# Kernel tuning notes

Hardware: AMD Instinct MI355X
Metric: run time of the kernel (lower is better)

The kernel has to match this reference:

```python
import jax, jax.numpy as jnp
import numpy as np

B, NUM_FRAMES, NUM_PATCHES = 2, 16, 196
DIM, H, DH = 768, 12, 64
T = NUM_FRAMES * NUM_PATCHES  # 3136
EPS = 1e-5


def setup_inputs() -> dict:
    key = jax.random.key(0)
    ks = jax.random.split(key, 5)
    x = jax.random.normal(ks[0], (B, T, DIM), jnp.float32)
    context = jax.random.normal(ks[1], (B, T, DIM), jnp.float32)
    Wq = jax.random.normal(ks[2], (DIM, H * DH), jnp.float32) * 0.02
    Wkv = jax.random.normal(ks[3], (DIM, 2 * H * DH), jnp.float32) * 0.02
    Wo = jax.random.normal(ks[4], (H * DH, DIM), jnp.float32) * 0.02
    bo = jnp.zeros((DIM,), jnp.float32)
    gamma = jnp.ones((DIM,), jnp.float32)
    beta = jnp.zeros((DIM,), jnp.float32)
    # block-diagonal frame mask: patch i attends to patch j iff same frame
    frame_ids = jnp.arange(T) // NUM_PATCHES
    mask = frame_ids[:, None] == frame_ids[None, :]  # [T, T] bool
    return {"x": x, "context": context, "Wq": Wq, "Wkv": Wkv, "Wo": Wo,
            "bo": bo, "gamma": gamma, "beta": beta, "mask": mask}


def reference(x, context, Wq, Wkv, Wo, bo, gamma, beta, mask):
    # LayerNorm on queries only (torch LN: biased variance, eps=1e-5)
    mu = jnp.mean(x, axis=-1, keepdims=True)
    var = jnp.var(x, axis=-1, keepdims=True)
    xn = (x - mu) * jax.lax.rsqrt(var + EPS) * gamma + beta

    q = xn @ Wq                      # [B, T, H*DH]
    kv = context @ Wkv               # [B, T, 2*H*DH]
    k, v = jnp.split(kv, 2, axis=-1)

    def split_heads(t):
        return t.reshape(B, T, H, DH).transpose(0, 2, 1, 3)  # [B, H, T, DH]

    q, k, v = split_heads(q), split_heads(k), split_heads(v)

    scale = DH ** -0.5
    dots = jnp.einsum('bhnd,bhmd->bhnm', q, k) * scale      # [B, H, T, T]
    dots = jnp.where(mask, dots, -jnp.inf)
    attn = jax.nn.softmax(dots, axis=-1)                    # dropout p=0.0 -> identity
    out = jnp.einsum('bhnm,bhmd->bhnd', attn, v)            # [B, H, T, DH]
    out = out.transpose(0, 2, 1, 3).reshape(B, T, H * DH)
    return out @ Wo + bo
```

## Files before the change

kernel.cpp:

```cpp
#include <hip/hip_runtime.h>
#include <hip/hip_bf16.h>

#define NB 2
#define TT 3136
#define DIM 768
#define NH 12
#define NF 16
#define NP 196

typedef __attribute__((ext_vector_type(8))) short short8;
typedef __attribute__((ext_vector_type(4))) short s16x4;
typedef __attribute__((ext_vector_type(4))) float f32x4;
typedef unsigned int uint;

__device__ __forceinline__ float bf2f(short s) {
    return __uint_as_float(((uint)(unsigned short)s) << 16);
}
__device__ __forceinline__ short f2bs(float f) {
    __hip_bfloat16 h = __float2bfloat16(f);
    short s; __builtin_memcpy(&s, &h, 2); return s;
}
__device__ __forceinline__ void load16_lds(const void* g, void* l) {
    __builtin_amdgcn_global_load_lds(
        (const __attribute__((address_space(1))) unsigned int*)g,
        (__attribute__((address_space(3))) unsigned int*)l, 16, 0, 0);
}

__global__ __launch_bounds__(256)
void prep_w(const float* __restrict__ Wq, const float* __restrict__ Wkv,
            const float* __restrict__ Wo,
            __hip_bfloat16* __restrict__ WqT, __hip_bfloat16* __restrict__ WkvT,
            __hip_bfloat16* __restrict__ WoT) {
    __shared__ float tile[32][33];
    int bx = blockIdx.x;
    const float* W; __hip_bfloat16* WT; int N, n0;
    if (bx < 24)      { W = Wq;  WT = WqT;  N = DIM;     n0 = bx * 32; }
    else if (bx < 72) { W = Wkv; WT = WkvT; N = 2 * DIM; n0 = (bx - 24) * 32; }
    else              { W = Wo;  WT = WoT;  N = DIM;     n0 = (bx - 72) * 32; }
    int k0 = blockIdx.y * 32;
    int tx = threadIdx.x & 31, ty = threadIdx.x >> 5;
#pragma unroll
    for (int i = 0; i < 32; i += 8)
        tile[ty + i][tx] = W[(size_t)(k0 + ty + i) * N + (n0 + tx)];
    __syncthreads();
#pragma unroll
    for (int i = 0; i < 32; i += 8)
        WT[(size_t)(n0 + ty + i) * DIM + (k0 + tx)] = __float2bfloat16(tile[tx][ty + i]);
}

__global__ __launch_bounds__(256)
void prep_xc(const float* __restrict__ ctx, __hip_bfloat16* __restrict__ cb,
             const float* __restrict__ x, const float* __restrict__ gamma,
             const float* __restrict__ beta, __hip_bfloat16* __restrict__ xn) {
    int blk = blockIdx.x, tid = threadIdx.x;
    if (blk < 4704) {
        size_t i = (size_t)blk * 256 + tid;
        f32x4 f; __builtin_memcpy(&f, ctx + i * 4, 16);
        s16x4 s;
#pragma unroll
        for (int j = 0; j < 4; j++) s[j] = f2bs(f[j]);
        __builtin_memcpy((short*)cb + i * 4, &s, 8);
        return;
    }
    int row = blk - 4704;
    const float* xr = x + (size_t)row * DIM;
    float v[3], s = 0.f, ss = 0.f;
#pragma unroll
    for (int i = 0; i < 3; i++) {
        v[i] = xr[tid + i * 256];
        s += v[i]; ss += v[i] * v[i];
    }
#pragma unroll
    for (int off = 32; off; off >>= 1) {
        s += __shfl_xor(s, off);
        ss += __shfl_xor(ss, off);
    }
    __shared__ float red[8];
    int wid = tid >> 6, lane = tid & 63;
    if (lane == 0) { red[wid] = s; red[wid + 4] = ss; }
    __syncthreads();
    if (tid == 0) {
        float S = red[0] + red[1] + red[2] + red[3];
        float SS = red[4] + red[5] + red[6] + red[7];
        float mu = S / DIM;
        float var = SS / DIM - mu * mu;
        red[0] = mu;
        red[1] = rsqrtf(var + 1e-5f);
    }
    __syncthreads();
    float mu = red[0], rs = red[1];
#pragma unroll
    for (int i = 0; i < 3; i++) {
        int c = tid + i * 256;
        xn[(size_t)row * DIM + c] = __float2bfloat16((v[i] - mu) * rs * gamma[c] + beta[c]);
    }
}

__global__ __launch_bounds__(256)
void gemm_qkv(const __hip_bfloat16* __restrict__ xn,
              const __hip_bfloat16* __restrict__ cb,
              const __hip_bfloat16* __restrict__ WqT,
              const __hip_bfloat16* __restrict__ WkvT,
              __hip_bfloat16* __restrict__ qbuf,
              __hip_bfloat16* __restrict__ kvbuf) {
    __shared__ short sA[2][128 * 64];
    __shared__ short sB[2][128 * 64];
    int orig = blockIdx.x;
    int xcd = orig & 7, pos = orig >> 3;
    int wgid = (xcd < 2 ? xcd * 111 : 222 + (xcd - 2) * 110) + pos;
    int mt = wgid / 18, nt = wgid - mt * 18;
    const __hip_bfloat16 *A, *BT;
    __hip_bfloat16* C;
    int N, n0;
    if (nt < 6) { A = xn; BT = WqT;  C = qbuf;  N = DIM;     n0 = nt * 128; }
    else        { A = cb; BT = WkvT; C = kvbuf; N = 2 * DIM; n0 = (nt - 6) * 128; }
    int m0 = mt * 128;
    int tid = threadIdx.x, lane = tid & 63, wave = tid >> 6;
    int r = lane & 15, q = lane >> 4;
    int wm = (wave & 1) * 64, wn = (wave >> 1) * 64;
    f32x4 acc[4][4] = {};

    auto stage = [&](int buf, int k0) {
#pragma unroll
        for (int i = 0; i < 4; i++) {
            int c = i * 256 + tid;
            int row = c >> 3, cg = c & 7;
            load16_lds(A + (size_t)(m0 + row) * DIM + k0 + cg * 8, &sA[buf][c * 8]);
        }
#pragma unroll
        for (int i = 0; i < 4; i++) {
            int c = i * 256 + tid;
            int row = c >> 3, cg = c & 7;
            load16_lds(BT + (size_t)(n0 + row) * DIM + k0 + cg * 8, &sB[buf][c * 8]);
        }
    };
    auto compute = [&](int buf) {
#pragma unroll
        for (int ks = 0; ks < 2; ks++) {
            short8 af[4], bfv[4];
#pragma unroll
            for (int t = 0; t < 4; t++) {
                __builtin_memcpy(&af[t],  &sA[buf][(wm + t * 16 + r) * 64 + ks * 32 + q * 8], 16);
                __builtin_memcpy(&bfv[t], &sB[buf][(wn + t * 16 + r) * 64 + ks * 32 + q * 8], 16);
            }
            __builtin_amdgcn_s_setprio(1);
#pragma unroll
            for (int mi = 0; mi < 4; mi++)
#pragma unroll
                for (int ni = 0; ni < 4; ni++)
                    acc[mi][ni] = __builtin_amdgcn_mfma_f32_16x16x32_bf16(
                        af[mi], bfv[ni], acc[mi][ni], 0, 0, 0);
            __builtin_amdgcn_s_setprio(0);
        }
    };

    stage(0, 0);
    __syncthreads();
    int cur = 0;
#pragma unroll 2
    for (int t = 0; t < 11; ++t) {
        stage(cur ^ 1, (t + 1) * 64);
        compute(cur);
        __syncthreads();
        cur ^= 1;
    }
    compute(cur);

#pragma unroll
    for (int mi = 0; mi < 4; mi++)
#pragma unroll
        for (int ni = 0; ni < 4; ni++)
#pragma unroll
            for (int rr = 0; rr < 4; rr++) {
                int row = m0 + wm + mi * 16 + q * 4 + rr;
                int col = n0 + wn + ni * 16 + r;
                C[(size_t)row * N + col] = __float2bfloat16(acc[mi][ni][rr]);
            }
}

__global__ __launch_bounds__(256)
void gemm_o(const __hip_bfloat16* __restrict__ A,
            const __hip_bfloat16* __restrict__ BT,
            const float* __restrict__ bias,
            float* __restrict__ C) {
    __shared__ short sA[2][128 * 64];
    __shared__ short sB[2][128 * 64];
    int orig = blockIdx.x;
    int xcd = orig & 7, pos = orig >> 3;
    int wgid = (xcd < 6 ? xcd * 37 : 222 + (xcd - 6) * 36) + pos;
    int mt = wgid / 6, nt = wgid - mt * 6;
    int m0 = mt * 128, n0 = nt * 128;
    int tid = threadIdx.x, lane = tid & 63, wave = tid >> 6;
    int r = lane & 15, q = lane >> 4;
    int wm = (wave & 1) * 64, wn = (wave >> 1) * 64;
    f32x4 acc[4][4] = {};

    auto stage = [&](int buf, int k0) {
#pragma unroll
        for (int i = 0; i < 4; i++) {
            int c = i * 256 + tid;
            int row = c >> 3, cg = c & 7;
            load16_lds(A + (size_t)(m0 + row) * DIM + k0 + cg * 8, &sA[buf][c * 8]);
        }
#pragma unroll
        for (int i = 0; i < 4; i++) {
            int c = i * 256 + tid;
            int row = c >> 3, cg = c & 7;
            load16_lds(BT + (size_t)(n0 + row) * DIM + k0 + cg * 8, &sB[buf][c * 8]);
        }
    };
    auto compute = [&](int buf) {
#pragma unroll
        for (int ks = 0; ks < 2; ks++) {
            short8 af[4], bfv[4];
#pragma unroll
            for (int t = 0; t < 4; t++) {
                __builtin_memcpy(&af[t],  &sA[buf][(wm + t * 16 + r) * 64 + ks * 32 + q * 8], 16);
                __builtin_memcpy(&bfv[t], &sB[buf][(wn + t * 16 + r) * 64 + ks * 32 + q * 8], 16);
            }
            __builtin_amdgcn_s_setprio(1);
#pragma unroll
            for (int mi = 0; mi < 4; mi++)
#pragma unroll
                for (int ni = 0; ni < 4; ni++)
                    acc[mi][ni] = __builtin_amdgcn_mfma_f32_16x16x32_bf16(
                        af[mi], bfv[ni], acc[mi][ni], 0, 0, 0);
            __builtin_amdgcn_s_setprio(0);
        }
    };

    stage(0, 0);
    __syncthreads();
    int cur = 0;
#pragma unroll 2
    for (int t = 0; t < 11; ++t) {
        stage(cur ^ 1, (t + 1) * 64);
        compute(cur);
        __syncthreads();
        cur ^= 1;
    }
    compute(cur);

    float bv[4];
#pragma unroll
    for (int ni = 0; ni < 4; ni++) bv[ni] = bias[n0 + wn + ni * 16 + r];
#pragma unroll
    for (int mi = 0; mi < 4; mi++)
#pragma unroll
        for (int ni = 0; ni < 4; ni++)
#pragma unroll
            for (int rr = 0; rr < 4; rr++) {
                int row = m0 + wm + mi * 16 + q * 4 + rr;
                int col = n0 + wn + ni * 16 + r;
                C[(size_t)row * DIM + col] = acc[mi][ni][rr] + bv[ni];
            }
}

__global__ __launch_bounds__(448)
void attn_kernel(__hip_bfloat16* qo,
                 const __hip_bfloat16* __restrict__ kvb) {
    __shared__ short sQ[112 * 66];
    __shared__ short sK[208 * 66];
    __shared__ short sVT[64 * 226];
    int blk = blockIdx.x;
    int half = blk & 1;
    int rest = blk >> 1;
    int f = rest % NF, h = (rest / NF) % NH, b = rest / (NF * NH);
    size_t tok0 = (size_t)b * TT + (size_t)f * NP;
    int row0 = half * 98;
    int tid = threadIdx.x, wave = tid >> 6, lane = tid & 63;
    int r = lane & 15, q = lane >> 4;

    for (int e = tid; e < 896; e += 448) {
        int row = e >> 3, cg = e & 7;
        short8 t = {0,0,0,0,0,0,0,0};
        if (row < 98)
            __builtin_memcpy(&t, qo + (tok0 + row0 + row) * DIM + h * 64 + cg * 8, 16);
        __builtin_memcpy(&sQ[row * 66 + cg * 8], &t, 16);
    }
    for (int e = tid; e < 1664; e += 448) {
        int row = e >> 3, cg = e & 7;
        short8 t = {0,0,0,0,0,0,0,0};
        if (row < NP)
            __builtin_memcpy(&t, kvb + (tok0 + row) * 1536 + h * 64 + cg * 8, 16);
        __builtin_memcpy(&sK[row * 66 + cg * 8], &t, 16);
    }
    for (int jj = 0; jj < 224; jj += 28) {
        int j = jj + (tid >> 4);
        int d = (tid & 15) * 4;
        s16x4 v = {0, 0, 0, 0};
        if (j < NP)
            __builtin_memcpy(&v, kvb + (tok0 + j) * 1536 + DIM + h * 64 + d, 8);
#pragma unroll
        for (int i = 0; i < 4; i++) sVT[(d + i) * 226 + j] = v[i];
    }
    __syncthreads();

    f32x4 sacc[13];
    short8 qf0, qf1;
    __builtin_memcpy(&qf0, &sQ[(wave * 16 + r) * 66 + q * 8], 16);
    __builtin_memcpy(&qf1, &sQ[(wave * 16 + r) * 66 + 32 + q * 8], 16);
#pragma unroll
    for (int jf = 0; jf < 13; jf++) {
        f32x4 a = {};
        short8 kf;
        __builtin_memcpy(&kf, &sK[(jf * 16 + r) * 66 + q * 8], 16);
        a = __builtin_amdgcn_mfma_f32_16x16x32_bf16(kf, qf0, a, 0, 0, 0);
        __builtin_memcpy(&kf, &sK[(jf * 16 + r) * 66 + 32 + q * 8], 16);
        a = __builtin_amdgcn_mfma_f32_16x16x32_bf16(kf, qf1, a, 0, 0, 0);
        sacc[jf] = a;
    }

    const float scale = 0.125f;
    float mx = -INFINITY;
#pragma unroll
    for (int jf = 0; jf < 13; jf++)
#pragma unroll
        for (int rg = 0; rg < 4; rg++) {
            bool valid = (jf < 12) | (q == 0);
            if (valid) mx = fmaxf(mx, sacc[jf][rg] * scale);
        }
    mx = fmaxf(mx, __shfl_xor(mx, 16));
    mx = fmaxf(mx, __shfl_xor(mx, 32));
    float ps = 0.f;
#pragma unroll
    for (int jf = 0; jf < 13; jf++)
#pragma unroll
        for (int rg = 0; rg < 4; rg++) {
            bool valid = (jf < 12) | (q == 0);
            float p = valid ? __expf(sacc[jf][rg] * scale - mx) : 0.f;
            sacc[jf][rg] = p;
            ps += p;
        }
    ps += __shfl_xor(ps, 16);
    ps += __shfl_xor(ps, 32);
    float inv = 1.f / ps;

    int srcl[8];
#pragma unroll
    for (int e = 0; e < 8; e++)
        srcl[e] = ((((q * 8 + e) >> 2) & 3) << 4) | r;
    short8 pa[7];
#pragma unroll
    for (int c = 0; c < 7; c++) {
#pragma unroll
        for (int e = 0; e < 8; e++) {
            float v0 = __shfl(sacc[2 * c][e & 3], srcl[e], 64);
            float v1 = (c < 6) ? __shfl(sacc[2 * c + 1][e & 3], srcl[e], 64) : 0.f;
            float val = (q >= 2) ? v1 : v0;
            pa[c][e] = f2bs(val * inv);
        }
    }

#pragma unroll
    for (int nt = 0; nt < 4; nt++) {
        f32x4 oacc = {};
#pragma unroll
        for (int kc = 0; kc < 7; kc++) {
            short8 bfv;
            __builtin_memcpy(&bfv, &sVT[(nt * 16 + r) * 226 + kc * 32 + q * 8], 16);
            oacc = __builtin_amdgcn_mfma_f32_16x16x32_bf16(pa[kc], bfv, oacc, 0, 0, 0);
        }
#pragma unroll
        for (int rg = 0; rg < 4; rg++) {
            int local = wave * 16 + q * 4 + rg;
            if (local < 98)
                qo[(tok0 + row0 + local) * DIM + h * 64 + nt * 16 + r] =
                    __float2bfloat16(oacc[rg]);
        }
    }
}

extern "C" void kernel_launch(void* const* d_in, const int* in_sizes, int n_in,
                              void* d_out, int out_size, void* d_ws, size_t ws_size,
                              hipStream_t stream) {
    const float* x     = (const float*)d_in[0];
    const float* ctx   = (const float*)d_in[1];
    const float* Wq    = (const float*)d_in[2];
    const float* Wkv   = (const float*)d_in[3];
    const float* Wo    = (const float*)d_in[4];
    const float* bo    = (const float*)d_in[5];
    const float* gamma = (const float*)d_in[6];
    const float* beta  = (const float*)d_in[7];

    char* ws = (char*)d_ws;
    __hip_bfloat16* cbuf  = (__hip_bfloat16*)(ws + 0);
    __hip_bfloat16* kvbuf = (__hip_bfloat16*)(ws + 9633792);
    __hip_bfloat16* qbuf  = (__hip_bfloat16*)(ws + 28901376);
    __hip_bfloat16* WqT   = (__hip_bfloat16*)(ws + 38535168);
    __hip_bfloat16* WkvT  = (__hip_bfloat16*)(ws + 39714816);
    __hip_bfloat16* WoT   = (__hip_bfloat16*)(ws + 42074112);
    __hip_bfloat16* xnbuf = (__hip_bfloat16*)d_out;
    float*          out   = (float*)d_out;

    prep_w<<<dim3(96, 24), 256, 0, stream>>>(Wq, Wkv, Wo, WqT, WkvT, WoT);
    prep_xc<<<10976, 256, 0, stream>>>(ctx, cbuf, x, gamma, beta, xnbuf);
    gemm_qkv<<<882, 256, 0, stream>>>(xnbuf, cbuf, WqT, WkvT, qbuf, kvbuf);
    attn_kernel<<<NB * NH * NF * 2, 448, 0, stream>>>(qbuf, kvbuf);
    gemm_o<<<294, 256, 0, stream>>>(qbuf, WoT, bo, out);
}
```

Before: 205.3 us.

## Use 256x256 tiles with 8 waves and swizzled LDS in QKV GEMM

```diff
diff --git a/kernel.cpp b/kernel.cpp
--- a/kernel.cpp
+++ b/kernel.cpp
@@ -96,85 +96,120 @@
     }
 }
 
-__global__ __launch_bounds__(256)
+__global__ __launch_bounds__(512, 1)
 void gemm_qkv(const __hip_bfloat16* __restrict__ xn,
               const __hip_bfloat16* __restrict__ cb,
               const __hip_bfloat16* __restrict__ WqT,
               const __hip_bfloat16* __restrict__ WkvT,
               __hip_bfloat16* __restrict__ qbuf,
               __hip_bfloat16* __restrict__ kvbuf) {
-    __shared__ short sA[2][128 * 64];
-    __shared__ short sB[2][128 * 64];
+    __shared__ short lds[2][2][2][8192];
+
     int orig = blockIdx.x;
     int xcd = orig & 7, pos = orig >> 3;
-    int wgid = (xcd < 2 ? xcd * 111 : 222 + (xcd - 2) * 110) + pos;
-    int mt = wgid / 18, nt = wgid - mt * 18;
-    const __hip_bfloat16 *A, *BT;
-    __hip_bfloat16* C;
+    int wgid = (xcd < 1 ? xcd * 29 : 29 + (xcd - 1) * 28) + pos;
+    int mt = wgid / 9, nt = wgid - mt * 9;
+
+    const __hip_bfloat16 *Abase, *Bbase; __hip_bfloat16* Cbase;
     int N, n0;
-    if (nt < 6) { A = xn; BT = WqT;  C = qbuf;  N = DIM;     n0 = nt * 128; }
-    else        { A = cb; BT = WkvT; C = kvbuf; N = 2 * DIM; n0 = (nt - 6) * 128; }
-    int m0 = mt * 128;
+    if (nt < 3) { Abase = xn; Bbase = WqT;  Cbase = qbuf;  N = DIM;  n0 = nt * 256; }
+    else        { Abase = cb; Bbase = WkvT; Cbase = kvbuf; N = 1536; n0 = (nt - 3) * 256; }
+    int m0 = mt * 256;
+
     int tid = threadIdx.x, lane = tid & 63, wave = tid >> 6;
     int r = lane & 15, q = lane >> 4;
-    int wm = (wave & 1) * 64, wn = (wave >> 1) * 64;
-    f32x4 acc[4][4] = {};
-
-    auto stage = [&](int buf, int k0) {
-#pragma unroll
-        for (int i = 0; i < 4; i++) {
-            int c = i * 256 + tid;
-            int row = c >> 3, cg = c & 7;
-            load16_lds(A + (size_t)(m0 + row) * DIM + k0 + cg * 8, &sA[buf][c * 8]);
-        }
-#pragma unroll
-        for (int i = 0; i < 4; i++) {
-            int c = i * 256 + tid;
-            int row = c >> 3, cg = c & 7;
-            load16_lds(BT + (size_t)(n0 + row) * DIM + k0 + cg * 8, &sB[buf][c * 8]);
-        }
+    int wm = wave >> 2, wn = wave & 3;
+    f32x4 acc[8][4] = {};
+
+    auto stageK = [&](int buf, int kt) {
+        int k0 = kt * 64;
+#pragma unroll
+        for (int h = 0; h < 2; h++)
+#pragma unroll
+            for (int s = 0; s < 2; s++) {
+                int idx = s * 512 + tid;
+                int row = idx >> 3, cg = idx & 7;
+                int w = (cg << 4) ^ ((row & 7) << 4);
+                int grow = m0 + h * 128 + row;
+                if (grow > TT * NB - 1) grow = TT * NB - 1;
+                load16_lds((const char*)Abase + ((size_t)grow * DIM + k0) * 2 + w,
+                           (char*)&lds[buf][0][h][0] + idx * 16);
+            }
+#pragma unroll
+        for (int h = 0; h < 2; h++)
+#pragma unroll
+            for (int s = 0; s < 2; s++) {
+                int idx = s * 512 + tid;
+                int row = idx >> 3, cg = idx & 7;
+                int w = (cg << 4) ^ ((row & 7) << 4);
+                int grow = n0 + h * 128 + row;
+                load16_lds((const char*)Bbase + ((size_t)grow * DIM + k0) * 2 + w,
+                           (char*)&lds[buf][1][h][0] + idx * 16);
+            }
     };
-    auto compute = [&](int buf) {
-#pragma unroll
-        for (int ks = 0; ks < 2; ks++) {
-            short8 af[4], bfv[4];
-#pragma unroll
-            for (int t = 0; t < 4; t++) {
-                __builtin_memcpy(&af[t],  &sA[buf][(wm + t * 16 + r) * 64 + ks * 32 + q * 8], 16);
-                __builtin_memcpy(&bfv[t], &sB[buf][(wn + t * 16 + r) * 64 + ks * 32 + q * 8], 16);
-            }
+
+    auto read_frag = [&](const char* base, int frag, int ks) {
+        short8 v;
+        int row_ = frag * 16 + r;
+        int byte_ = row_ * 128 + ((ks * 64 + q * 16) ^ ((r & 7) << 4));
+        __builtin_memcpy(&v, base + byte_, 16);
+        return v;
+    };
+
+    stageK(0, 0);
+    asm volatile("s_waitcnt vmcnt(0)" ::: "memory");
+    __builtin_amdgcn_s_barrier();
+
+    for (int t = 0; t < 12; ++t) {
+        int cur = t & 1;
+        const char* Ah = (const char*)&lds[cur][0][wm][0];
+        const char* Bh = (const char*)&lds[cur][1][wn >> 1][0];
+        int bbase = (wn & 1) * 4;
+        short8 breg[4][2];
+#pragma unroll
+        for (int p = 0; p < 4; p++) {
+            short8 areg[2][2];
+#pragma unroll
+            for (int i = 0; i < 2; i++)
+#pragma unroll
+                for (int ks = 0; ks < 2; ks++)
+                    areg[i][ks] = read_frag(Ah, p * 2 + i, ks);
+            if (p == 0) {
+#pragma unroll
+                for (int n = 0; n < 4; n++)
+#pragma unroll
+                    for (int ks = 0; ks < 2; ks++)
+                        breg[n][ks] = read_frag(Bh, bbase + n, ks);
+                if (t < 11) stageK(cur ^ 1, t + 1);
+            }
+            __builtin_amdgcn_s_barrier();
             __builtin_amdgcn_s_setprio(1);
 #pragma unroll
-            for (int mi = 0; mi < 4; mi++)
-#pragma unroll
-                for (int ni = 0; ni < 4; ni++)
-                    acc[mi][ni] = __builtin_amdgcn_mfma_f32_16x16x32_bf16(
-                        af[mi], bfv[ni], acc[mi][ni], 0, 0, 0);
+            for (int i = 0; i < 2; i++)
+#pragma unroll
+                for (int n = 0; n < 4; n++)
+#pragma unroll
+                    for (int ks = 0; ks < 2; ks++)
+                        acc[p * 2 + i][n] = __builtin_amdgcn_mfma_f32_16x16x32_bf16(
+                            areg[i][ks], breg[n][ks], acc[p * 2 + i][n], 0, 0, 0);
             __builtin_amdgcn_s_setprio(0);
-        }
-    };
-
-    stage(0, 0);
-    __syncthreads();
-    int cur = 0;
-#pragma unroll 2
-    for (int t = 0; t < 11; ++t) {
-        stage(cur ^ 1, (t + 1) * 64);
-        compute(cur);
-        __syncthreads();
-        cur ^= 1;
-    }
-    compute(cur);
-
-#pragma unroll
-    for (int mi = 0; mi < 4; mi++)
-#pragma unroll
-        for (int ni = 0; ni < 4; ni++)
+            if (p == 3)
+                asm volatile("s_waitcnt vmcnt(0)" ::: "memory");
+            __builtin_amdgcn_s_barrier();
+        }
+    }
+
+#pragma unroll
+    for (int mf = 0; mf < 8; mf++)
+#pragma unroll
+        for (int n = 0; n < 4; n++)
 #pragma unroll
             for (int rr = 0; rr < 4; rr++) {
-                int row = m0 + wm + mi * 16 + q * 4 + rr;
-                int col = n0 + wn + ni * 16 + r;
-                C[(size_t)row * N + col] = __float2bfloat16(acc[mi][ni][rr]);
+                int row = m0 + wm * 128 + mf * 16 + q * 4 + rr;
+                if (row < TT * NB) {
+                    int col = n0 + wn * 64 + n * 16 + r;
+                    Cbase[(size_t)row * N + col] = __float2bfloat16(acc[mf][n][rr]);
+                }
             }
 }
 
@@ -395,7 +430,7 @@
 
     prep_w<<<dim3(96, 24), 256, 0, stream>>>(Wq, Wkv, Wo, WqT, WkvT, WoT);
     prep_xc<<<10976, 256, 0, stream>>>(ctx, cbuf, x, gamma, beta, xnbuf);
-    gemm_qkv<<<882, 256, 0, stream>>>(xnbuf, cbuf, WqT, WkvT, qbuf, kvbuf);
+    gemm_qkv<<<225, 512, 0, stream>>>(xnbuf, cbuf, WqT, WkvT, qbuf, kvbuf);
     attn_kernel<<<NB * NH * NF * 2, 448, 0, stream>>>(qbuf, kvbuf);
     gemm_o<<<294, 256, 0, stream>>>(qbuf, WoT, bo, out);
 }
```

New measurement: 202.1 us. No clear change (-1.6%).
